# Kernel tuning notes

Measured on AMD Instinct MI355X. Metric: run time of the kernel, lower is better.

## Reference

```python
import jax, jax.numpy as jnp
import numpy as np

B, L, H, NH = 4, 1024, 768, 12      # docs, seq len, hidden, attn heads
E, M, P = 30, 8, 512                # entities/doc, mentions/entity, ht pairs/doc
NLAB = 97                           # DocRED relation count
EMB, BLK = 768, 64                  # emb_size, block_size
OFFSET = 1                          # bert cls offset


def setup_inputs() -> dict:
    key = jax.random.key(0)
    ks = jax.random.split(key, 24)
    def n(k, shp, s=0.02):
        return jax.random.normal(k, shp, jnp.float32) * s
    seq_out = jax.random.normal(ks[0], (B, L, H), jnp.float32)
    attn = jax.random.uniform(ks[1], (B, NH, L, L), jnp.float32)
    mention_idx = jax.random.randint(ks[2], (B, E, M), 0, L - 2)
    ht_pairs = jax.random.randint(ks[3], (B, P, 2), 0, E)
    label_emb = jax.random.normal(ks[4], (NLAB, H), jnp.float32)
    adj = (jax.random.uniform(ks[5], (NLAB, NLAB)) < 0.2).astype(jnp.int32)
    label_adj = jnp.maximum(adj, jnp.eye(NLAB, dtype=jnp.int32))  # self loops
    return dict(
        seq_out=seq_out, attn=attn, mention_idx=mention_idx, ht_pairs=ht_pairs,
        label_adj=label_adj, label_emb=label_emb,
        gW0=n(ks[6], (H, 2 * 500)), gal0=n(ks[7], (2, 500)), gar0=n(ks[8], (2, 500)),
        gW1=n(ks[9], (1000, 2 * 500)), gal1=n(ks[10], (2, 500)), gar1=n(ks[11], (2, 500)),
        gW2=n(ks[12], (1000, H)), gal2=n(ks[13], (1, H)), gar2=n(ks[14], (1, H)),
        ln_gamma=jnp.ones((NLAB,), jnp.float32), ln_beta=jnp.zeros((NLAB,), jnp.float32),
        W_lin2=n(ks[15], (2 * NLAB, NLAB)), b_lin2=jnp.zeros((NLAB,), jnp.float32),
        W_head=n(ks[16], (2 * H, EMB)), b_head=jnp.zeros((EMB,), jnp.float32),
        W_tail=n(ks[17], (2 * H, EMB)), b_tail=jnp.zeros((EMB,), jnp.float32),
        W_bil=n(ks[18], (EMB * BLK + NLAB, NLAB)), b_bil=jnp.zeros((NLAB,), jnp.float32),
    )


def _gat_layer(x, W, al, ar, adj, act):
    nh, od = al.shape
    z = (x @ W).reshape(x.shape[0], nh, od)          # [N, nh, od]
    el = (z * al[None]).sum(-1)                      # src scores [N, nh]
    er = (z * ar[None]).sum(-1)                      # dst scores [N, nh]
    e = jax.nn.leaky_relu(er[:, None, :] + el[None, :, :], 0.2)  # [dst, src, nh]
    e = jnp.where((adj.T > 0)[:, :, None], e, -1e9)
    a = jax.nn.softmax(e, axis=1)
    out = jnp.einsum('vuh,uhd->vhd', a, z)
    return act(out) if act is not None else out


def _layer_norm(x, g, b, eps=1e-5):
    m = x.mean(-1, keepdims=True)
    v = ((x - m) ** 2).mean(-1, keepdims=True)
    return (x - m) * jax.lax.rsqrt(v + eps) * g + b


def _forward(seq_out, attn, label_emb, gW0, gal0, gar0, gW1, gal1, gar1,
             gW2, gal2, gar2, ln_gamma, ln_beta, W_lin2, b_lin2,
             W_head, b_head, W_tail, b_tail, W_bil, b_bil,
             mention_idx, ht_pairs, label_adj):
    pos = mention_idx + OFFSET                                   # [B,E,M]
    bidx3 = jnp.arange(B)[:, None, None]
    ment_emb = seq_out[bidx3, pos]                               # [B,E,M,H]
    ent_emb = jax.nn.logsumexp(ment_emb, axis=2)                 # [B,E,H]
    ment_att = attn[bidx3, :, pos]                               # [B,E,M,NH,L]
    ent_att = ment_att.mean(2)                                   # [B,E,NH,L]

    bidx2 = jnp.arange(B)[:, None]
    h_idx, t_idx = ht_pairs[..., 0], ht_pairs[..., 1]            # [B,P]
    hs = ent_emb[bidx2, h_idx]                                   # [B,P,H]
    ts = ent_emb[bidx2, t_idx]
    ht_att = (ent_att[bidx2, h_idx] * ent_att[bidx2, t_idx]).mean(2)  # [B,P,L]
    ht_att = ht_att / (ht_att.sum(-1, keepdims=True) + 1e-5)
    rs = jnp.einsum('bld,brl->brd', seq_out, ht_att)             # [B,P,H]

    N = B * P
    hs, ts, rs = hs.reshape(N, H), ts.reshape(N, H), rs.reshape(N, H)

    # label GAT: 2 hidden layers (2 heads, concat) + output head
    x = _gat_layer(label_emb, gW0, gal0, gar0, label_adj, None).reshape(NLAB, -1)
    x = jax.nn.elu(x)
    x = _gat_layer(x, gW1, gal1, gar1, label_adj, None).reshape(NLAB, -1)
    x = jax.nn.elu(x)
    lab = _gat_layer(x, gW2, gal2, gar2, label_adj, None).reshape(NLAB, H)

    hs_li = _layer_norm(hs @ lab.T, ln_gamma, ln_beta)           # [N,97]
    ts_li = _layer_norm(ts @ lab.T, ln_gamma, ln_beta)
    logits_li = jnp.concatenate([hs_li, ts_li], axis=1) @ W_lin2 + b_lin2

    hs2 = jnp.tanh(jnp.concatenate([hs, rs], axis=1) @ W_head + b_head)
    ts2 = jnp.tanh(jnp.concatenate([ts, rs], axis=1) @ W_tail + b_tail)
    b1 = hs2.reshape(N, EMB // BLK, BLK)
    b2 = ts2.reshape(N, EMB // BLK, BLK)
    bl = (b1[:, :, :, None] * b2[:, :, None, :]).reshape(N, EMB * BLK)
    logits = jnp.concatenate([bl, logits_li], axis=1) @ W_bil + b_bil
    return logits


def reference(seq_out, attn, mention_idx, ht_pairs, label_adj, label_emb,
              gW0, gal0, gar0, gW1, gal1, gar1, gW2, gal2, gar2,
              ln_gamma, ln_beta, W_lin2, b_lin2, W_head, b_head,
              W_tail, b_tail, W_bil, b_bil):
    return _forward(seq_out, attn, label_emb, gW0, gal0, gar0, gW1, gal1, gar1,
                    gW2, gal2, gar2, ln_gamma, ln_beta, W_lin2, b_lin2,
                    W_head, b_head, W_tail, b_tail, W_bil, b_bil,
                    mention_idx, ht_pairs, label_adj)
```

## Files before the change

### kernel.cpp

```cpp
#include <hip/hip_runtime.h>
#include <hip/hip_bf16.h>
#include <math.h>

typedef __hip_bfloat16 bf16;

__device__ __forceinline__ float toF(float x){ return x; }
__device__ __forceinline__ float toF(bf16 x){ return __bfloat162float(x); }
__device__ __forceinline__ void storeF(float v, float* p){ *p = v; }
__device__ __forceinline__ void storeF(float v, bf16* p){ *p = __float2bfloat16(v); }

__device__ __forceinline__ float bfLo(unsigned u){ return __uint_as_float(u << 16); }
__device__ __forceinline__ float bfHi(unsigned u){ return __uint_as_float(u & 0xFFFF0000u); }

__device__ __forceinline__ bool gateOff(const int* flag, int want){
    return flag && (*flag != want);
}

__global__ void detect_kernel(const unsigned int* gamma_bits, int* flag){
    if (threadIdx.x == 0) *flag = (gamma_bits[0] == 0x3F800000u) ? 0 : 1;
}

template<typename T>
__global__ void cvt_in(const T* __restrict__ in, float* __restrict__ out, int n,
                       const int* flag, int want){
    if (gateOff(flag, want)) return;
    int i = blockIdx.x*256 + threadIdx.x;
    if (i < n) out[i] = toF(in[i]);
}

template<typename T>
__global__ void store_out(const float* __restrict__ in, T* __restrict__ out, int n,
                          const int* flag, int want){
    if (gateOff(flag, want)) return;
    int i = blockIdx.x*256 + threadIdx.x;
    if (i < n) storeF(in[i], &out[i]);
}

template<typename T>
__global__ void ent_emb_kernel(const T* __restrict__ seq, const int* __restrict__ midx,
                               float* __restrict__ ent_emb, const int* flag, int want){
    if (gateOff(flag, want)) return;
    int be = blockIdx.x;
    int b  = be / 30;
    __shared__ int pos[8];
    if (threadIdx.x < 8) pos[threadIdx.x] = midx[be*8 + threadIdx.x] + 1;
    __syncthreads();
    for (int h = threadIdx.x; h < 768; h += 256){
        float v[8], mx = -1e30f;
        #pragma unroll
        for (int m=0;m<8;m++){
            v[m] = toF(seq[((size_t)b*1024 + pos[m])*768 + h]);
            mx = fmaxf(mx, v[m]);
        }
        float s = 0.f;
        #pragma unroll
        for (int m=0;m<8;m++) s += __expf(v[m]-mx);
        ent_emb[(size_t)be*768 + h] = mx + __logf(s);
    }
}

template<typename T>
__global__ void ent_att_kernel(const T* __restrict__ attn, const int* __restrict__ midx,
                               float* __restrict__ ent_att, const int* flag, int want){
    if (gateOff(flag, want)) return;
    int id = blockIdx.x;
    int nh = id % 12, be = id / 12, b = be / 30;
    __shared__ int pos[8];
    if (threadIdx.x < 8) pos[threadIdx.x] = midx[be*8 + threadIdx.x] + 1;
    __syncthreads();
    const size_t base = ((size_t)(b*12 + nh))*1024*1024;
    for (int l = threadIdx.x; l < 1024; l += 256){
        float s = 0.f;
        #pragma unroll
        for (int m=0;m<8;m++) s += toF(attn[base + (size_t)pos[m]*1024 + l]);
        ent_att[((size_t)be*12 + nh)*1024 + l] = s * 0.125f;
    }
}

__global__ void pair_kernel(const float* __restrict__ ent_emb, const float* __restrict__ ent_att,
                            const int* __restrict__ htp,
                            float* __restrict__ hs, float* __restrict__ ts, float* __restrict__ ht_att){
    int n = blockIdx.x;
    int b = n >> 9;
    int h = htp[n*2], t = htp[n*2+1];
    const float* eh = ent_emb + ((size_t)b*30 + h)*768;
    const float* et = ent_emb + ((size_t)b*30 + t)*768;
    for (int d = threadIdx.x; d < 768; d += 256){
        hs[(size_t)n*768 + d] = eh[d];
        ts[(size_t)n*768 + d] = et[d];
    }
    const float* ah = ent_att + ((size_t)b*30 + h)*12*1024;
    const float* at = ent_att + ((size_t)b*30 + t)*12*1024;
    float loc[4]; float psum = 0.f;
    #pragma unroll
    for (int i=0;i<4;i++){
        int l = threadIdx.x + i*256;
        float s = 0.f;
        #pragma unroll
        for (int k=0;k<12;k++) s += ah[k*1024 + l]*at[k*1024 + l];
        s *= (1.f/12.f);
        loc[i] = s; psum += s;
    }
    __shared__ float red[256];
    red[threadIdx.x] = psum; __syncthreads();
    for (int off=128; off>0; off>>=1){
        if (threadIdx.x < off) red[threadIdx.x] += red[threadIdx.x+off];
        __syncthreads();
    }
    float inv = 1.f/(red[0] + 1e-5f);
    #pragma unroll
    for (int i=0;i<4;i++){
        int l = threadIdx.x + i*256;
        ht_att[(size_t)n*1024 + l] = loc[i]*inv;
    }
}

template<typename T>
__global__ void rs_kernel(const T* __restrict__ seq, const float* __restrict__ ht_att,
                          float* __restrict__ rs, const int* flag, int want){
    if (gateOff(flag, want)) return;
    int hc = blockIdx.x;
    int pt = blockIdx.y;
    int b  = blockIdx.z;
    int h  = hc*256 + threadIdx.x;
    float acc[16];
    #pragma unroll
    for (int i=0;i<16;i++) acc[i]=0.f;
    __shared__ __align__(16) float att[64][20];
    for (int l0=0; l0<1024; l0+=64){
        for (int idx=threadIdx.x; idx<1024; idx+=256){
            int pl = idx>>6, lo = idx&63;
            att[lo][pl] = ht_att[((size_t)(b*512 + pt*16 + pl))*1024 + l0 + lo];
        }
        __syncthreads();
        for (int lo=0; lo<64; lo++){
            float sv = toF(seq[((size_t)b*1024 + l0 + lo)*768 + h]);
            #pragma unroll
            for (int p=0;p<16;p++) acc[p] += att[lo][p]*sv;
        }
        __syncthreads();
    }
    #pragma unroll
    for (int p=0;p<16;p++)
        rs[((size_t)(b*512 + pt*16 + p))*768 + h] = acc[p];
}

template<typename TB>
__global__ __launch_bounds__(256) void gemm64(const float* __restrict__ A1, const float* __restrict__ A2,
                                              int K1, int K, const TB* __restrict__ B,
                                              const TB* __restrict__ bias, int act,
                                              float* __restrict__ C, int M, int N,
                                              const int* flag, int want){
    if (gateOff(flag, want)) return;
    __shared__ __align__(16) float As[32][68];
    __shared__ __align__(16) float Bs[32][68];
    int m0 = blockIdx.y*64, n0 = blockIdx.x*64;
    int tid = threadIdx.x;
    int tr = tid>>4, tc = tid&15;
    float acc[4][4];
    #pragma unroll
    for (int i=0;i<4;i++)
        #pragma unroll
        for (int j=0;j<4;j++) acc[i][j]=0.f;
    int K2 = K - K1;
    for (int k0=0; k0<K; k0+=32){
        for (int e=tid; e<2048; e+=256){
            int k=e&31, m=e>>5;
            int gm=m0+m, gk=k0+k;
            float v=0.f;
            if (gm<M && gk<K) v = (gk<K1)? A1[(size_t)gm*K1+gk] : A2[(size_t)gm*K2 + (gk-K1)];
            As[k][m]=v;
        }
        for (int e=tid; e<2048; e+=256){
            int nn=e&63, k=e>>6;
            int gk=k0+k, gn=n0+nn;
            float v=0.f;
            if (gk<K && gn<N) v = toF(B[(size_t)gk*N+gn]);
            Bs[k][nn]=v;
        }
        __syncthreads();
        #pragma unroll
        for (int kk=0;kk<32;kk++){
            float4 a4 = *(const float4*)&As[kk][tr<<2];
            float4 b4 = *(const float4*)&Bs[kk][tc<<2];
            float av[4]={a4.x,a4.y,a4.z,a4.w}, bv[4]={b4.x,b4.y,b4.z,b4.w};
            #pragma unroll
            for (int i=0;i<4;i++)
                #pragma unroll
                for (int j=0;j<4;j++) acc[i][j] += av[i]*bv[j];
        }
        __syncthreads();
    }
    #pragma unroll
    for (int i=0;i<4;i++){
        int m = m0 + (tr<<2) + i;
        if (m >= M) continue;
        #pragma unroll
        for (int j=0;j<4;j++){
            int n = n0 + (tc<<2) + j;
            if (n >= N) continue;
            float v = acc[i][j];
            if (bias) v += toF(bias[n]);
            if (act == 1) v = tanhf(v);
            C[(size_t)m*N + n] = v;
        }
    }
}

template<typename T>
__global__ void elr_kernel(const float* __restrict__ z, const T* __restrict__ al,
                           const T* __restrict__ ar, int nh, int od,
                           float* __restrict__ el, float* __restrict__ er,
                           const int* flag, int want){
    if (gateOff(flag, want)) return;
    int u = blockIdx.x;
    __shared__ float sl[256], sr[256];
    int tid = threadIdx.x;
    for (int h=0; h<nh; h++){
        float a=0.f, r=0.f;
        for (int d=tid; d<od; d+=256){
            float zz = z[((size_t)u*nh + h)*od + d];
            a += zz*toF(al[h*od+d]);
            r += zz*toF(ar[h*od+d]);
        }
        sl[tid]=a; sr[tid]=r; __syncthreads();
        for (int off=128; off>0; off>>=1){
            if (tid<off){ sl[tid]+=sl[tid+off]; sr[tid]+=sr[tid+off]; }
            __syncthreads();
        }
        if (tid==0){ el[u*nh+h]=sl[0]; er[u*nh+h]=sr[0]; }
        __syncthreads();
    }
}

__global__ void gat_agg_kernel(const float* __restrict__ z, const float* __restrict__ el,
                               const float* __restrict__ er, const int* __restrict__ adj,
                               int nh, int od, int applyElu, float* __restrict__ out){
    int v = blockIdx.x;
    int tid = threadIdx.x;
    __shared__ float e[2][97];
    int D = nh*od;
    for (int idx=tid; idx<97*nh; idx+=256){
        int u = idx % 97, h = idx / 97;
        float ev;
        if (adj[u*97 + v] > 0){
            ev = er[v*nh+h] + el[u*nh+h];
            ev = ev > 0.f ? ev : 0.2f*ev;
        } else ev = -1e9f;
        e[h][u] = ev;
    }
    __syncthreads();
    if (tid < nh){
        float mx=-1e30f;
        for (int u2=0;u2<97;u2++) mx = fmaxf(mx, e[tid][u2]);
        float s=0.f;
        for (int u2=0;u2<97;u2++){ float x=__expf(e[tid][u2]-mx); e[tid][u2]=x; s+=x; }
        float inv = 1.f/s;
        for (int u2=0;u2<97;u2++) e[tid][u2]*=inv;
    }
    __syncthreads();
    for (int d0=tid; d0<D; d0+=256){
        int h = d0 / od;
        float s = 0.f;
        for (int u2=0;u2<97;u2++) s += e[h][u2]*z[(size_t)u2*D + d0];
        if (applyElu) s = s>0.f ? s : expm1f(s);
        out[(size_t)v*D + d0] = s;
    }
}

__global__ void transpose_kernel(const float* __restrict__ lab, float* __restrict__ labT){
    int i = blockIdx.x*256 + threadIdx.x;
    if (i < 97*768){ int c = i/768, k = i%768; labT[(size_t)k*97 + c] = lab[i]; }
}

template<typename T>
__global__ void ln_kernel(const float* __restrict__ in, const T* __restrict__ gamma,
                          const T* __restrict__ beta, float* __restrict__ out,
                          const int* flag, int want){
    if (gateOff(flag, want)) return;
    int n = blockIdx.x;
    int tid = threadIdx.x;
    __shared__ float red[128];
    float v = (tid < 97) ? in[(size_t)n*97 + tid] : 0.f;
    red[tid] = v; __syncthreads();
    for (int off=64; off>0; off>>=1){
        if (tid<off) red[tid]+=red[tid+off];
        __syncthreads();
    }
    float mean = red[0]*(1.f/97.f); __syncthreads();
    float d = (tid < 97) ? v - mean : 0.f;
    red[tid] = d*d; __syncthreads();
    for (int off=64; off>0; off>>=1){
        if (tid<off) red[tid]+=red[tid+off];
        __syncthreads();
    }
    float rstd = rsqrtf(red[0]*(1.f/97.f) + 1e-5f);
    if (tid < 97)
        out[(size_t)n*97 + tid] = d*rstd*toF(gamma[tid]) + toF(beta[tid]);
}

template<typename T>
__global__ __launch_bounds__(256) void bilinear_kernel(const float* __restrict__ hs2,
                                                       const float* __restrict__ ts2,
                                                       const T* __restrict__ Wb,
                                                       float* __restrict__ out,
                                                       const int* flag, int want){
    if (gateOff(flag, want)) return;
    int nb = blockIdx.x, g = blockIdx.y, ih = blockIdx.z;
    int n0 = nb*32;
    __shared__ __align__(16) float hsb[16][36];
    __shared__ __align__(16) float tsb[64][36];
    __shared__ __align__(16) float wbuf[2][3104];
    int tid = threadIdx.x;
    for (int e=tid; e<512; e+=256){
        int i = e&15, nl = e>>4;
        hsb[i][nl] = hs2[(size_t)(n0+nl)*768 + g*64 + ih*16 + i];
    }
    for (int e=tid; e<2048; e+=256){
        int j = e&63, nl = e>>6;
        tsb[j][nl] = ts2[(size_t)(n0+nl)*768 + g*64 + j];
    }
    const T* Wg = Wb + (size_t)g*4096*97 + (size_t)ih*16*6208;

    if constexpr (sizeof(T) == 4){
        const float4* src = (const float4*)Wg;
        float4* dst = (float4*)wbuf[0];
        #pragma unroll
        for (int u=0;u<4;u++){ int e = tid + u*256; if (e < 776) dst[e] = src[e]; }
    } else {
        const uint4* src = (const uint4*)Wg;
        #pragma unroll
        for (int u=0;u<2;u++){
            int e = tid + u*256;
            if (e < 388){
                uint4 w = src[e];
                float* d = &wbuf[0][e*8];
                d[0]=bfLo(w.x); d[1]=bfHi(w.x); d[2]=bfLo(w.y); d[3]=bfHi(w.y);
                d[4]=bfLo(w.z); d[5]=bfHi(w.z); d[6]=bfLo(w.w); d[7]=bfHi(w.w);
            }
        }
    }
    __syncthreads();

    int cg = tid & 63;
    int ng = tid >> 6;
    int c0 = cg, c1 = cg + 64;
    bool c1ok = (c1 < 97);
    float acc0[8], acc1[8];
    #pragma unroll
    for (int q=0;q<8;q++){ acc0[q]=0.f; acc1[q]=0.f; }

    int cur = 0;
    for (int k=0; k<32; ++k){
        int i = k>>1;
        float4 wreg[4];
        uint4  breg[2];
        if (k+1 < 32){
            if constexpr (sizeof(T) == 4){
                const float4* src = (const float4*)(Wg + (size_t)(k+1)*3104);
                #pragma unroll
                for (int u=0;u<4;u++){ int e = tid + u*256; if (e < 776) wreg[u] = src[e]; }
            } else {
                const uint4* src = (const uint4*)(Wg + (size_t)(k+1)*3104);
                #pragma unroll
                for (int u=0;u<2;u++){ int e = tid + u*256; if (e < 388) breg[u] = src[e]; }
            }
        }
        float a[8];
        #pragma unroll
        for (int q=0;q<8;q++) a[q] = hsb[i][ng*8+q];
        float s0[8], s1[8];
        #pragma unroll
        for (int q=0;q<8;q++){ s0[q]=0.f; s1[q]=0.f; }
        const float* wrow = wbuf[cur];
        int jbase = (k&1)*32;
        #pragma unroll 2
        for (int j=0;j<32;j++){
            float w0 = wrow[j*97 + c0];
            float w1 = c1ok ? wrow[j*97 + c1] : 0.f;
            const float4* tp = (const float4*)&tsb[jbase + j][ng*8];
            float4 t0 = tp[0], t1 = tp[1];
            float tv[8] = {t0.x,t0.y,t0.z,t0.w,t1.x,t1.y,t1.z,t1.w};
            #pragma unroll
            for (int q=0;q<8;q++){ s0[q] += tv[q]*w0; s1[q] += tv[q]*w1; }
        }
        #pragma unroll
        for (int q=0;q<8;q++){ acc0[q] += a[q]*s0[q]; acc1[q] += a[q]*s1[q]; }
        if (k+1 < 32){
            if constexpr (sizeof(T) == 4){
                float4* dst = (float4*)wbuf[cur^1];
                #pragma unroll
                for (int u=0;u<4;u++){ int e = tid + u*256; if (e < 776) dst[e] = wreg[u]; }
            } else {
                float* base = wbuf[cur^1];
                #pragma unroll
                for (int u=0;u<2;u++){
                    int e = tid + u*256;
                    if (e < 388){
                        uint4 w = breg[u];
                        float* d = &base[e*8];
                        d[0]=bfLo(w.x); d[1]=bfHi(w.x); d[2]=bfLo(w.y); d[3]=bfHi(w.y);
                        d[4]=bfLo(w.z); d[5]=bfHi(w.z); d[6]=bfLo(w.w); d[7]=bfHi(w.w);
                    }
                }
            }
        }
        __syncthreads();
        cur ^= 1;
    }
    #pragma unroll
    for (int q=0;q<8;q++){
        int n = n0 + ng*8 + q;
        atomicAdd(&out[(size_t)n*97 + c0], acc0[q]);
        if (c1ok) atomicAdd(&out[(size_t)n*97 + c1], acc1[q]);
    }
}

extern "C" void kernel_launch(void* const* d_in, const int* in_sizes, int n_in,
                              void* d_out, int out_size, void* d_ws, size_t ws_size,
                              hipStream_t stream){
    (void)in_sizes; (void)n_in; (void)ws_size; (void)out_size;
    const void* seq   = d_in[0];
    const void* attn  = d_in[1];
    const int*  midx  = (const int*)d_in[2];
    const int*  htp   = (const int*)d_in[3];
    const int*  adj   = (const int*)d_in[4];
    const void* lemb  = d_in[5];
    const void* gW0   = d_in[6];
    const void* gal0  = d_in[7];
    const void* gar0  = d_in[8];
    const void* gW1   = d_in[9];
    const void* gal1  = d_in[10];
    const void* gar1  = d_in[11];
    const void* gW2   = d_in[12];
    const void* gal2  = d_in[13];
    const void* gar2  = d_in[14];
    const void* ln_g  = d_in[15];
    const void* ln_b  = d_in[16];
    const void* Wlin2 = d_in[17];
    const void* blin2 = d_in[18];
    const void* Whead = d_in[19];
    const void* bhead = d_in[20];
    const void* Wtail = d_in[21];
    const void* btail = d_in[22];
    const void* Wbil  = d_in[23];
    const void* bbil  = d_in[24];

    int*   flag = (int*)d_ws;
    float* base = (float*)d_ws + 16;
    float* hs     = base;
    float* ts     = hs + 1572864;
    float* R2     = ts + 1572864;
    float* ht_att = R2;
    float* hs2    = R2;
    float* li_raw = R2 + 1572864;
    float* R3     = R2 + 2097152;
    float* ent_emb= R3;
    float* ent_att= R3 + 92160;
    float* li     = R3;
    float* ts2    = R3;
    float* rs     = R3 + 1572864;
    float* sm     = rs + 1572864;
    float* x0   = sm;
    float* zbuf = x0 + 74496;
    float* x1   = zbuf + 97000;
    float* x2   = x1 + 97000;
    float* lab  = x2 + 97000;
    float* labT = lab + 74496;
    float* el   = labT + 74496;
    float* er   = el + 194;
    float* ll   = er + 194;
    float* logits = ll + 198656;

    detect_kernel<<<1,64,0,stream>>>((const unsigned int*)ln_g, flag);

    ent_emb_kernel<float><<<120,256,0,stream>>>((const float*)seq, midx, ent_emb, flag, 0);
    ent_emb_kernel<bf16 ><<<120,256,0,stream>>>((const bf16* )seq, midx, ent_emb, flag, 1);
    ent_att_kernel<float><<<1440,256,0,stream>>>((const float*)attn, midx, ent_att, flag, 0);
    ent_att_kernel<bf16 ><<<1440,256,0,stream>>>((const bf16* )attn, midx, ent_att, flag, 1);
    pair_kernel<<<2048,256,0,stream>>>(ent_emb, ent_att, htp, hs, ts, ht_att);
    rs_kernel<float><<<dim3(3,32,4),256,0,stream>>>((const float*)seq, ht_att, rs, flag, 0);
    rs_kernel<bf16 ><<<dim3(3,32,4),256,0,stream>>>((const bf16* )seq, ht_att, rs, flag, 1);

    cvt_in<float><<<(74496+255)/256,256,0,stream>>>((const float*)lemb, x0, 74496, flag, 0);
    cvt_in<bf16 ><<<(74496+255)/256,256,0,stream>>>((const bf16* )lemb, x0, 74496, flag, 1);

    auto gemm_pair = [&](const float* A1, const float* A2, int K1, int K,
                         const void* B, const void* bias, int act,
                         float* C, int M, int N, dim3 grid){
        gemm64<float><<<grid,256,0,stream>>>(A1,A2,K1,K,(const float*)B,(const float*)bias,act,C,M,N,flag,0);
        gemm64<bf16 ><<<grid,256,0,stream>>>(A1,A2,K1,K,(const bf16* )B,(const bf16* )bias,act,C,M,N,flag,1);
    };
    auto elr_pair = [&](const float* z, const void* al, const void* ar, int nh, int od){
        elr_kernel<float><<<97,256,0,stream>>>(z,(const float*)al,(const float*)ar,nh,od,el,er,flag,0);
        elr_kernel<bf16 ><<<97,256,0,stream>>>(z,(const bf16* )al,(const bf16* )ar,nh,od,el,er,flag,1);
    };

    gemm_pair(x0, nullptr, 768, 768, gW0, nullptr, 0, zbuf, 97, 1000, dim3(16,2));
    elr_pair(zbuf, gal0, gar0, 2, 500);
    gat_agg_kernel<<<97,256,0,stream>>>(zbuf, el, er, adj, 2, 500, 1, x1);
    gemm_pair(x1, nullptr, 1000, 1000, gW1, nullptr, 0, zbuf, 97, 1000, dim3(16,2));
    elr_pair(zbuf, gal1, gar1, 2, 500);
    gat_agg_kernel<<<97,256,0,stream>>>(zbuf, el, er, adj, 2, 500, 1, x2);
    gemm_pair(x2, nullptr, 1000, 1000, gW2, nullptr, 0, zbuf, 97, 768, dim3(12,2));
    elr_pair(zbuf, gal2, gar2, 1, 768);
    gat_agg_kernel<<<97,256,0,stream>>>(zbuf, el, er, adj, 1, 768, 0, lab);
    transpose_kernel<<<(74496+255)/256,256,0,stream>>>(lab, labT);

    gemm64<float><<<dim3(2,64),256,0,stream>>>(hs, nullptr, 768, 768, labT,
        (const float*)nullptr, 0, li_raw, 4096, 97, nullptr, 0);
    ln_kernel<float><<<4096,128,0,stream>>>(li_raw, (const float*)ln_g, (const float*)ln_b, li, flag, 0);
    ln_kernel<bf16 ><<<4096,128,0,stream>>>(li_raw, (const bf16* )ln_g, (const bf16* )ln_b, li, flag, 1);
    gemm_pair(li, li + 2048*97, 97, 194, Wlin2, blin2, 0, ll, 2048, 97, dim3(2,32));

    gemm_pair(hs, rs, 768, 1536, Whead, bhead, 1, hs2, 2048, 768, dim3(12,32));
    gemm_pair(ts, rs, 768, 1536, Wtail, btail, 1, ts2, 2048, 768, dim3(12,32));

    gemm64<float><<<dim3(2,32),256,0,stream>>>(ll, nullptr, 97, 97,
        (const float*)Wbil + (size_t)49152*97, (const float*)bbil, 0, logits, 2048, 97, flag, 0);
    gemm64<bf16 ><<<dim3(2,32),256,0,stream>>>(ll, nullptr, 97, 97,
        (const bf16* )Wbil + (size_t)49152*97, (const bf16* )bbil, 0, logits, 2048, 97, flag, 1);

    bilinear_kernel<float><<<dim3(64,12,4),256,0,stream>>>(hs2, ts2, (const float*)Wbil, logits, flag, 0);
    bilinear_kernel<bf16 ><<<dim3(64,12,4),256,0,stream>>>(hs2, ts2, (const bf16* )Wbil, logits, flag, 1);

    store_out<float><<<(198656+255)/256,256,0,stream>>>(logits, (float*)d_out, 198656, flag, 0);
    store_out<bf16 ><<<(198656+255)/256,256,0,stream>>>(logits, (bf16*)d_out, 198656, flag, 1);
}
```

Before: 2.623 ms.

## Compute head/tail and label projections per entity, merge dtype kernel pairs

Because hs and ts are gathers of per-entity embeddings, the entity-side parts of the head/tail GEMMs and the label-interaction GEMM plus LayerNorm and lin2 are now computed once per entity (120 rows) rather than per pair (2048 or 4096 rows). Per-pair results are then assembled by gathering them, either in the GEMM epilogue (a new act==2 path that adds the gathered entity term before tanh) or in a small ll kernel. The separate float and bf16 kernel launches are also merged into single kernels that branch on the dtype flag at runtime. This removes redundant FLOPs, the hs/ts materialization and about half of the launches, in exchange for more code size and a possible register-pressure increase from instantiating both templates in each kernel.

```diff
diff --git a/kernel.cpp b/kernel.cpp
--- a/kernel.cpp
+++ b/kernel.cpp
@@ -6,89 +6,90 @@
 
 __device__ __forceinline__ float toF(float x){ return x; }
 __device__ __forceinline__ float toF(bf16 x){ return __bfloat162float(x); }
-__device__ __forceinline__ void storeF(float v, float* p){ *p = v; }
-__device__ __forceinline__ void storeF(float v, bf16* p){ *p = __float2bfloat16(v); }
 
 __device__ __forceinline__ float bfLo(unsigned u){ return __uint_as_float(u << 16); }
 __device__ __forceinline__ float bfHi(unsigned u){ return __uint_as_float(u & 0xFFFF0000u); }
 
-__device__ __forceinline__ bool gateOff(const int* flag, int want){
-    return flag && (*flag != want);
-}
+__device__ __forceinline__ int rdFlag(const int* flag){ return flag ? *flag : 0; }
 
 __global__ void detect_kernel(const unsigned int* gamma_bits, int* flag){
     if (threadIdx.x == 0) *flag = (gamma_bits[0] == 0x3F800000u) ? 0 : 1;
 }
 
 template<typename T>
-__global__ void cvt_in(const T* __restrict__ in, float* __restrict__ out, int n,
-                       const int* flag, int want){
-    if (gateOff(flag, want)) return;
+__device__ __forceinline__ void cvt_core(const T* in, float* out, int n){
     int i = blockIdx.x*256 + threadIdx.x;
     if (i < n) out[i] = toF(in[i]);
 }
-
-template<typename T>
-__global__ void store_out(const float* __restrict__ in, T* __restrict__ out, int n,
-                          const int* flag, int want){
-    if (gateOff(flag, want)) return;
+__global__ void cvt_in_m(const void* in, float* __restrict__ out, int n, const int* flag){
+    if (!rdFlag(flag)) cvt_core<float>((const float*)in, out, n);
+    else               cvt_core<bf16 >((const bf16* )in, out, n);
+}
+
+template<typename T>
+__device__ __forceinline__ void store_core(const float* in, T* out, int n){
     int i = blockIdx.x*256 + threadIdx.x;
-    if (i < n) storeF(in[i], &out[i]);
-}
-
-template<typename T>
-__global__ void ent_emb_kernel(const T* __restrict__ seq, const int* __restrict__ midx,
-                               float* __restrict__ ent_emb, const int* flag, int want){
-    if (gateOff(flag, want)) return;
-    int be = blockIdx.x;
-    int b  = be / 30;
+    if (i < n) out[i] = (sizeof(T)==4) ? (T)in[i] : (T)__float2bfloat16(in[i]);
+}
+__global__ void store_out_m(const float* __restrict__ in, void* out, int n, const int* flag){
+    if (!rdFlag(flag)){ int i = blockIdx.x*256 + threadIdx.x; if (i<n) ((float*)in, ((float*)out)[i] = in[i]); }
+    else              { int i = blockIdx.x*256 + threadIdx.x; if (i<n) ((bf16*)out)[i] = __float2bfloat16(in[i]); }
+}
+
+template<typename T>
+__device__ __forceinline__ void ent_emb_core(const T* seq, const int* pos, int b, int be,
+                                             float* ent_emb){
+    for (int h = threadIdx.x; h < 768; h += 256){
+        float v[8], mx = -1e30f;
+        #pragma unroll
+        for (int m=0;m<8;m++){
+            v[m] = toF(seq[((size_t)b*1024 + pos[m])*768 + h]);
+            mx = fmaxf(mx, v[m]);
+        }
+        float s = 0.f;
+        #pragma unroll
+        for (int m=0;m<8;m++) s += __expf(v[m]-mx);
+        ent_emb[(size_t)be*768 + h] = mx + __logf(s);
+    }
+}
+__global__ void ent_emb_m(const void* seq, const int* __restrict__ midx,
+                          float* __restrict__ ent_emb, const int* flag){
+    int be = blockIdx.x, b = be/30;
     __shared__ int pos[8];
     if (threadIdx.x < 8) pos[threadIdx.x] = midx[be*8 + threadIdx.x] + 1;
     __syncthreads();
-    for (int h = threadIdx.x; h < 768; h += 256){
-        float v[8], mx = -1e30f;
-        #pragma unroll
-        for (int m=0;m<8;m++){
-            v[m] = toF(seq[((size_t)b*1024 + pos[m])*768 + h]);
-            mx = fmaxf(mx, v[m]);
-        }
+    if (!rdFlag(flag)) ent_emb_core<float>((const float*)seq, pos, b, be, ent_emb);
+    else               ent_emb_core<bf16 >((const bf16* )seq, pos, b, be, ent_emb);
+}
+
+template<typename T>
+__device__ __forceinline__ void ent_att_core(const T* attn, const int* pos, size_t base,
+                                             int be, int nh, float* ent_att){
+    for (int l = threadIdx.x; l < 1024; l += 256){
         float s = 0.f;
         #pragma unroll
-        for (int m=0;m<8;m++) s += __expf(v[m]-mx);
-        ent_emb[(size_t)be*768 + h] = mx + __logf(s);
-    }
-}
-
-template<typename T>
-__global__ void ent_att_kernel(const T* __restrict__ attn, const int* __restrict__ midx,
-                               float* __restrict__ ent_att, const int* flag, int want){
-    if (gateOff(flag, want)) return;
+        for (int m=0;m<8;m++) s += toF(attn[base + (size_t)pos[m]*1024 + l]);
+        ent_att[((size_t)be*12 + nh)*1024 + l] = s * 0.125f;
+    }
+}
+__global__ void ent_att_m(const void* attn, const int* __restrict__ midx,
+                          float* __restrict__ ent_att, const int* flag){
     int id = blockIdx.x;
     int nh = id % 12, be = id / 12, b = be / 30;
     __shared__ int pos[8];
     if (threadIdx.x < 8) pos[threadIdx.x] = midx[be*8 + threadIdx.x] + 1;
     __syncthreads();
     const size_t base = ((size_t)(b*12 + nh))*1024*1024;
-    for (int l = threadIdx.x; l < 1024; l += 256){
-        float s = 0.f;
-        #pragma unroll
-        for (int m=0;m<8;m++) s += toF(attn[base + (size_t)pos[m]*1024 + l]);
-        ent_att[((size_t)be*12 + nh)*1024 + l] = s * 0.125f;
-    }
-}
-
-__global__ void pair_kernel(const float* __restrict__ ent_emb, const float* __restrict__ ent_att,
+    if (!rdFlag(flag)) ent_att_core<float>((const float*)attn, pos, base, be, nh, ent_att);
+    else               ent_att_core<bf16 >((const bf16* )attn, pos, base, be, nh, ent_att);
+}
+
+__global__ void pair_kernel(const float* __restrict__ ent_att,
                             const int* __restrict__ htp,
-                            float* __restrict__ hs, float* __restrict__ ts, float* __restrict__ ht_att){
+                            float* __restrict__ ht_att){
     int n = blockIdx.x;
     int b = n >> 9;
     int h = htp[n*2], t = htp[n*2+1];
-    const float* eh = ent_emb + ((size_t)b*30 + h)*768;
-    const float* et = ent_emb + ((size_t)b*30 + t)*768;
-    for (int d = threadIdx.x; d < 768; d += 256){
-        hs[(size_t)n*768 + d] = eh[d];
-        ts[(size_t)n*768 + d] = et[d];
-    }
     const float* ah = ent_att + ((size_t)b*30 + h)*12*1024;
     const float* at = ent_att + ((size_t)b*30 + t)*12*1024;
     float loc[4]; float psum = 0.f;
@@ -116,17 +117,13 @@
 }
 
 template<typename T>
-__global__ void rs_kernel(const T* __restrict__ seq, const float* __restrict__ ht_att,
-                          float* __restrict__ rs, const int* flag, int want){
-    if (gateOff(flag, want)) return;
-    int hc = blockIdx.x;
-    int pt = blockIdx.y;
-    int b  = blockIdx.z;
+__device__ __forceinline__ void rs_core(const T* seq, const float* ht_att, float* rs,
+                                        float (*att)[20]){
+    int hc = blockIdx.x, pt = blockIdx.y, b = blockIdx.z;
     int h  = hc*256 + threadIdx.x;
     float acc[16];
     #pragma unroll
     for (int i=0;i<16;i++) acc[i]=0.f;
-    __shared__ __align__(16) float att[64][20];
     for (int l0=0; l0<1024; l0+=64){
         for (int idx=threadIdx.x; idx<1024; idx+=256){
             int pl = idx>>6, lo = idx&63;
@@ -144,16 +141,19 @@
     for (int p=0;p<16;p++)
         rs[((size_t)(b*512 + pt*16 + p))*768 + h] = acc[p];
 }
+__global__ void rs_m(const void* seq, const float* __restrict__ ht_att,
+                     float* __restrict__ rs, const int* flag){
+    __shared__ __align__(16) float att[64][20];
+    if (!rdFlag(flag)) rs_core<float>((const float*)seq, ht_att, rs, att);
+    else               rs_core<bf16 >((const bf16* )seq, ht_att, rs, att);
+}
 
 template<typename TB>
-__global__ __launch_bounds__(256) void gemm64(const float* __restrict__ A1, const float* __restrict__ A2,
-                                              int K1, int K, const TB* __restrict__ B,
-                                              const TB* __restrict__ bias, int act,
-                                              float* __restrict__ C, int M, int N,
-                                              const int* flag, int want){
-    if (gateOff(flag, want)) return;
-    __shared__ __align__(16) float As[32][68];
-    __shared__ __align__(16) float Bs[32][68];
+__device__ __forceinline__ void gemm64_core(const float* A1, const float* A2,
+                                            int K1, int K, const TB* B, const TB* bias,
+                                            int act, float* C, int M, int N,
+                                            const float* addG, const int* htp, int sel,
+                                            float (*As)[68], float (*Bs)[68]){
     int m0 = blockIdx.y*64, n0 = blockIdx.x*64;
     int tid = threadIdx.x;
     int tr = tid>>4, tc = tid&15;
@@ -195,6 +195,8 @@
     for (int i=0;i<4;i++){
         int m = m0 + (tr<<2) + i;
         if (m >= M) continue;
+        int e2 = (act==2) ? htp[m*2+sel] : 0;
+        int bb = m >> 9;
         #pragma unroll
         for (int j=0;j<4;j++){
             int n = n0 + (tc<<2) + j;
@@ -202,19 +204,32 @@
             float v = acc[i][j];
             if (bias) v += toF(bias[n]);
             if (act == 1) v = tanhf(v);
+            else if (act == 2) v = tanhf(v + addG[(size_t)(bb*30+e2)*768 + n]);
             C[(size_t)m*N + n] = v;
         }
     }
 }
-
-template<typename T>
-__global__ void elr_kernel(const float* __restrict__ z, const T* __restrict__ al,
-                           const T* __restrict__ ar, int nh, int od,
-                           float* __restrict__ el, float* __restrict__ er,
-                           const int* flag, int want){
-    if (gateOff(flag, want)) return;
+__global__ __launch_bounds__(256) void gemm64_m(const float* __restrict__ A1,
+                                                const float* __restrict__ A2,
+                                                int K1, int K, const void* B, size_t boff,
+                                                const void* bias, int act,
+                                                float* __restrict__ C, int M, int N,
+                                                const int* flag,
+                                                const float* __restrict__ addG,
+                                                const int* __restrict__ htp, int sel){
+    __shared__ __align__(16) float As[32][68];
+    __shared__ __align__(16) float Bs[32][68];
+    if (!rdFlag(flag))
+        gemm64_core<float>(A1,A2,K1,K,(const float*)B + boff,(const float*)bias,act,C,M,N,addG,htp,sel,As,Bs);
+    else
+        gemm64_core<bf16 >(A1,A2,K1,K,(const bf16* )B + boff,(const bf16* )bias,act,C,M,N,addG,htp,sel,As,Bs);
+}
+
+template<typename T>
+__device__ __forceinline__ void elr_core(const float* z, const T* al, const T* ar,
+                                         int nh, int od, float* el, float* er,
+                                         float* sl, float* sr){
     int u = blockIdx.x;
-    __shared__ float sl[256], sr[256];
     int tid = threadIdx.x;
     for (int h=0; h<nh; h++){
         float a=0.f, r=0.f;
@@ -231,6 +246,13 @@
         if (tid==0){ el[u*nh+h]=sl[0]; er[u*nh+h]=sr[0]; }
         __syncthreads();
     }
+}
+__global__ void elr_m(const float* __restrict__ z, const void* al, const void* ar,
+                      int nh, int od, float* __restrict__ el, float* __restrict__ er,
+                      const int* flag){
+    __shared__ float sl[256], sr[256];
+    if (!rdFlag(flag)) elr_core<float>(z,(const float*)al,(const float*)ar,nh,od,el,er,sl,sr);
+    else               elr_core<bf16 >(z,(const bf16* )al,(const bf16* )ar,nh,od,el,er,sl,sr);
 }
 
 __global__ void gat_agg_kernel(const float* __restrict__ z, const float* __restrict__ el,
@@ -274,14 +296,11 @@
 }
 
 template<typename T>
-__global__ void ln_kernel(const float* __restrict__ in, const T* __restrict__ gamma,
-                          const T* __restrict__ beta, float* __restrict__ out,
-                          const int* flag, int want){
-    if (gateOff(flag, want)) return;
-    int n = blockIdx.x;
-    int tid = threadIdx.x;
-    __shared__ float red[128];
-    float v = (tid < 97) ? in[(size_t)n*97 + tid] : 0.f;
+__device__ __forceinline__ void p5_core(const float* EL, const T* g, const T* bta,
+                                        const T* W2, float* Eh2, float* Et2,
+                                        float* red, float* eln){
+    int e = blockIdx.x, tid = threadIdx.x;
+    float v = (tid < 97) ? EL[(size_t)e*97 + tid] : 0.f;
     red[tid] = v; __syncthreads();
     for (int off=64; off>0; off>>=1){
         if (tid<off) red[tid]+=red[tid+off];
@@ -295,22 +314,53 @@
         __syncthreads();
     }
     float rstd = rsqrtf(red[0]*(1.f/97.f) + 1e-5f);
-    if (tid < 97)
-        out[(size_t)n*97 + tid] = d*rstd*toF(gamma[tid]) + toF(beta[tid]);
-}
-
-template<typename T>
-__global__ __launch_bounds__(256) void bilinear_kernel(const float* __restrict__ hs2,
-                                                       const float* __restrict__ ts2,
-                                                       const T* __restrict__ Wb,
-                                                       float* __restrict__ out,
-                                                       const int* flag, int want){
-    if (gateOff(flag, want)) return;
+    if (tid < 97) eln[tid] = d*rstd*toF(g[tid]) + toF(bta[tid]);
+    __syncthreads();
+    if (tid < 97){
+        float s0=0.f, s1=0.f;
+        for (int k=0;k<97;k++){
+            float x = eln[k];
+            s0 += x*toF(W2[k*97 + tid]);
+            s1 += x*toF(W2[(k+97)*97 + tid]);
+        }
+        Eh2[(size_t)e*97 + tid] = s0;
+        Et2[(size_t)e*97 + tid] = s1;
+    }
+}
+__global__ void p5_m(const float* __restrict__ EL, const void* g, const void* bta,
+                     const void* W2, float* __restrict__ Eh2, float* __restrict__ Et2,
+                     const int* flag){
+    __shared__ float red[128];
+    __shared__ float eln[97];
+    if (!rdFlag(flag)) p5_core<float>(EL,(const float*)g,(const float*)bta,(const float*)W2,Eh2,Et2,red,eln);
+    else               p5_core<bf16 >(EL,(const bf16* )g,(const bf16* )bta,(const bf16* )W2,Eh2,Et2,red,eln);
+}
+
+template<typename T>
+__device__ __forceinline__ void ll_core(const float* Eh2, const float* Et2,
+                                        const int* htp, const T* blin2, float* ll){
+    int n = blockIdx.x;
+    int b = n >> 9;
+    int h = htp[n*2], t = htp[n*2+1];
+    int c = threadIdx.x;
+    if (c < 97)
+        ll[(size_t)n*97 + c] = Eh2[(size_t)(b*30+h)*97 + c]
+                             + Et2[(size_t)(b*30+t)*97 + c] + toF(blin2[c]);
+}
+__global__ void ll_m(const float* __restrict__ Eh2, const float* __restrict__ Et2,
+                     const int* __restrict__ htp, const void* blin2,
+                     float* __restrict__ ll, const int* flag){
+    if (!rdFlag(flag)) ll_core<float>(Eh2,Et2,htp,(const float*)blin2,ll);
+    else               ll_core<bf16 >(Eh2,Et2,htp,(const bf16* )blin2,ll);
+}
+
+template<typename T>
+__device__ __forceinline__ void bilinear_core(const float* hs2, const float* ts2,
+                                              const T* Wb, float* out,
+                                              float (*hsb)[36], float (*tsb)[36],
+                                              float (*wbuf)[3104]){
     int nb = blockIdx.x, g = blockIdx.y, ih = blockIdx.z;
     int n0 = nb*32;
-    __shared__ __align__(16) float hsb[16][36];
-    __shared__ __align__(16) float tsb[64][36];
-    __shared__ __align__(16) float wbuf[2][3104];
     int tid = threadIdx.x;
     for (int e=tid; e<512; e+=256){
         int i = e&15, nl = e>>4;
@@ -322,7 +372,7 @@
     }
     const T* Wg = Wb + (size_t)g*4096*97 + (size_t)ih*16*6208;
 
-    if constexpr (sizeof(T) == 4){
+    if (sizeof(T) == 4){
         const float4* src = (const float4*)Wg;
         float4* dst = (float4*)wbuf[0];
         #pragma unroll
@@ -356,7 +406,7 @@
         float4 wreg[4];
         uint4  breg[2];
         if (k+1 < 32){
-            if constexpr (sizeof(T) == 4){
+            if (sizeof(T) == 4){
                 const float4* src = (const float4*)(Wg + (size_t)(k+1)*3104);
                 #pragma unroll
                 for (int u=0;u<4;u++){ int e = tid + u*256; if (e < 776) wreg[u] = src[e]; }
@@ -387,7 +437,7 @@
         #pragma unroll
         for (int q=0;q<8;q++){ acc0[q] += a[q]*s0[q]; acc1[q] += a[q]*s1[q]; }
         if (k+1 < 32){
-            if constexpr (sizeof(T) == 4){
+            if (sizeof(T) == 4){
                 float4* dst = (float4*)wbuf[cur^1];
                 #pragma unroll
                 for (int u=0;u<4;u++){ int e = tid + u*256; if (e < 776) dst[e] = wreg[u]; }
@@ -414,6 +464,17 @@
         atomicAdd(&out[(size_t)n*97 + c0], acc0[q]);
         if (c1ok) atomicAdd(&out[(size_t)n*97 + c1], acc1[q]);
     }
+}
+__global__ __launch_bounds__(256) void bilinear_m(const float* __restrict__ hs2,
+                                                  const float* __restrict__ ts2,
+                                                  const void* Wb,
+                                                  float* __restrict__ out,
+                                                  const int* flag){
+    __shared__ __align__(16) float hsb[16][36];
+    __shared__ __align__(16) float tsb[64][36];
+    __shared__ __align__(16) float wbuf[2][3104];
+    if (!rdFlag(flag)) bilinear_core<float>(hs2, ts2, (const float*)Wb, out, hsb, tsb, wbuf);
+    else               bilinear_core<bf16 >(hs2, ts2, (const bf16* )Wb, out, hsb, tsb, wbuf);
 }
 
 extern "C" void kernel_launch(void* const* d_in, const int* in_sizes, int n_in,
@@ -448,19 +509,20 @@
 
     int*   flag = (int*)d_ws;
     float* base = (float*)d_ws + 16;
-    float* hs     = base;
-    float* ts     = hs + 1572864;
-    float* R2     = ts + 1572864;
+    float* EWh  = base;
+    float* EWt  = EWh + 92160;
+    float* EL   = EWt + 92160;
+    float* Eh2  = EL  + 11640;
+    float* Et2  = Eh2 + 11640;
+    float* R2     = base + 2*1572864;
     float* ht_att = R2;
     float* hs2    = R2;
-    float* li_raw = R2 + 1572864;
     float* R3     = R2 + 2097152;
     float* ent_emb= R3;
     float* ent_att= R3 + 92160;
-    float* li     = R3;
     float* ts2    = R3;
     float* rs     = R3 + 1572864;
-    float* sm     = rs + 1572864;
+    float* sm   = rs + 1572864;
     float* x0   = sm;
     float* zbuf = x0 + 74496;
     float* x1   = zbuf + 97000;
@@ -474,56 +536,45 @@
 
     detect_kernel<<<1,64,0,stream>>>((const unsigned int*)ln_g, flag);
 
-    ent_emb_kernel<float><<<120,256,0,stream>>>((const float*)seq, midx, ent_emb, flag, 0);
-    ent_emb_kernel<bf16 ><<<120,256,0,stream>>>((const bf16* )seq, midx, ent_emb, flag, 1);
-    ent_att_kernel<float><<<1440,256,0,stream>>>((const float*)attn, midx, ent_att, flag, 0);
-    ent_att_kernel<bf16 ><<<1440,256,0,stream>>>((const bf16* )attn, midx, ent_att, flag, 1);
-    pair_kernel<<<2048,256,0,stream>>>(ent_emb, ent_att, htp, hs, ts, ht_att);
-    rs_kernel<float><<<dim3(3,32,4),256,0,stream>>>((const float*)seq, ht_att, rs, flag, 0);
-    rs_kernel<bf16 ><<<dim3(3,32,4),256,0,stream>>>((const bf16* )seq, ht_att, rs, flag, 1);
-
-    cvt_in<float><<<(74496+255)/256,256,0,stream>>>((const float*)lemb, x0, 74496, flag, 0);
-    cvt_in<bf16 ><<<(74496+255)/256,256,0,stream>>>((const bf16* )lemb, x0, 74496, flag, 1);
-
-    auto gemm_pair = [&](const float* A1, const float* A2, int K1, int K,
-                         const void* B, const void* bias, int act,
-                         float* C, int M, int N, dim3 grid){
-        gemm64<float><<<grid,256,0,stream>>>(A1,A2,K1,K,(const float*)B,(const float*)bias,act,C,M,N,flag,0);
-        gemm64<bf16 ><<<grid,256,0,stream>>>(A1,A2,K1,K,(const bf16* )B,(const bf16* )bias,act,C,M,N,flag,1);
-    };
-    auto elr_pair = [&](const float* z, const void* al, const void* ar, int nh, int od){
-        elr_kernel<float><<<97,256,0,stream>>>(z,(const float*)al,(const float*)ar,nh,od,el,er,flag,0);
-        elr_kernel<bf16 ><<<97,256,0,stream>>>(z,(const bf16* )al,(const bf16* )ar,nh,od,el,er,flag,1);
-    };
-
-    gemm_pair(x0, nullptr, 768, 768, gW0, nullptr, 0, zbuf, 97, 1000, dim3(16,2));
-    elr_pair(zbuf, gal0, gar0, 2, 500);
+    ent_emb_m<<<120,256,0,stream>>>(seq, midx, ent_emb, flag);
+    ent_att_m<<<1440,256,0,stream>>>(attn, midx, ent_att, flag);
+    pair_kernel<<<2048,256,0,stream>>>(ent_att, htp, ht_att);
+    rs_m<<<dim3(3,32,4),256,0,stream>>>(seq, ht_att, rs, flag);
+
+    gemm64_m<<<dim3(12,2),256,0,stream>>>(ent_emb, nullptr, 768, 768, Whead, 0, bhead, 0,
+                                          EWh, 120, 768, flag, nullptr, nullptr, 0);
+    gemm64_m<<<dim3(12,2),256,0,stream>>>(ent_emb, nullptr, 768, 768, Wtail, 0, btail, 0,
+                                          EWt, 120, 768, flag, nullptr, nullptr, 0);
+
+    cvt_in_m<<<(74496+255)/256,256,0,stream>>>(lemb, x0, 74496, flag);
+
+    gemm64_m<<<dim3(16,2),256,0,stream>>>(x0, nullptr, 768, 768, gW0, 0, nullptr, 0,
+                                          zbuf, 97, 1000, flag, nullptr, nullptr, 0);
+    elr_m<<<97,256,0,stream>>>(zbuf, gal0, gar0, 2, 500, el, er, flag);
     gat_agg_kernel<<<97,256,0,stream>>>(zbuf, el, er, adj, 2, 500, 1, x1);
-    gemm_pair(x1, nullptr, 1000, 1000, gW1, nullptr, 0, zbuf, 97, 1000, dim3(16,2));
-    elr_pair(zbuf, gal1, gar1, 2, 500);
+    gemm64_m<<<dim3(16,2),256,0,stream>>>(x1, nullptr, 1000, 1000, gW1, 0, nullptr, 0,
+                                          zbuf, 97, 1000, flag, nullptr, nullptr, 0);
+    elr_m<<<97,256,0,stream>>>(zbuf, gal1, gar1, 2, 500, el, er, flag);
     gat_agg_kernel<<<97,256,0,stream>>>(zbuf, el, er, adj, 2, 500, 1, x2);
-    gemm_pair(x2, nullptr, 1000, 1000, gW2, nullptr, 0, zbuf, 97, 768, dim3(12,2));
-    elr_pair(zbuf, gal2, gar2, 1, 768);
+    gemm64_m<<<dim3(12,2),256,0,stream>>>(x2, nullptr, 1000, 1000, gW2, 0, nullptr, 0,
+                                          zbuf, 97, 768, flag, nullptr, nullptr, 0);
+    elr_m<<<97,256,0,stream>>>(zbuf, gal2, gar2, 1, 768, el, er, flag);
     gat_agg_kernel<<<97,256,0,stream>>>(zbuf, el, er, adj, 1, 768, 0, lab);
     transpose_kernel<<<(74496+255)/256,256,0,stream>>>(lab, labT);
 
-    gemm64<float><<<dim3(2,64),256,0,stream>>>(hs, nullptr, 768, 768, labT,
-        (const float*)nullptr, 0, li_raw, 4096, 97, nullptr, 0);
-    ln_kernel<float><<<4096,128,0,stream>>>(li_raw, (const float*)ln_g, (const float*)ln_b, li, flag, 0);
-    ln_kernel<bf16 ><<<4096,128,0,stream>>>(li_raw, (const bf16* )ln_g, (const bf16* )ln_b, li, flag, 1);
-    gemm_pair(li, li + 2048*97, 97, 194, Wlin2, blin2, 0, ll, 2048, 97, dim3(2,32));
-
-    gemm_pair(hs, rs, 768, 1536, Whead, bhead, 1, hs2, 2048, 768, dim3(12,32));
-    gemm_pair(ts, rs, 768, 1536, Wtail, btail, 1, ts2, 2048, 768, dim3(12,32));
-
-    gemm64<float><<<dim3(2,32),256,0,stream>>>(ll, nullptr, 97, 97,
-        (const float*)Wbil + (size_t)49152*97, (const float*)bbil, 0, logits, 2048, 97, flag, 0);
-    gemm64<bf16 ><<<dim3(2,32),256,0,stream>>>(ll, nullptr, 97, 97,
-        (const bf16* )Wbil + (size_t)49152*97, (const bf16* )bbil, 0, logits, 2048, 97, flag, 1);
-
-    bilinear_kernel<float><<<dim3(64,12,4),256,0,stream>>>(hs2, ts2, (const float*)Wbil, logits, flag, 0);
-    bilinear_kernel<bf16 ><<<dim3(64,12,4),256,0,stream>>>(hs2, ts2, (const bf16* )Wbil, logits, flag, 1);
-
-    store_out<float><<<(198656+255)/256,256,0,stream>>>(logits, (float*)d_out, 198656, flag, 0);
-    store_out<bf16 ><<<(198656+255)/256,256,0,stream>>>(logits, (bf16*)d_out, 198656, flag, 1);
-}
+    gemm64_m<<<dim3(2,2),256,0,stream>>>(ent_emb, nullptr, 768, 768, labT, 0, nullptr, 0,
+                                         EL, 120, 97, nullptr, nullptr, nullptr, 0);
+    p5_m<<<120,128,0,stream>>>(EL, ln_g, ln_b, Wlin2, Eh2, Et2, flag);
+    ll_m<<<2048,128,0,stream>>>(Eh2, Et2, htp, blin2, ll, flag);
+
+    gemm64_m<<<dim3(12,32),256,0,stream>>>(rs, nullptr, 768, 768, Whead, 589824, nullptr, 2,
+                                           hs2, 2048, 768, flag, EWh, htp, 0);
+    gemm64_m<<<dim3(12,32),256,0,stream>>>(rs, nullptr, 768, 768, Wtail, 589824, nullptr, 2,
+                                           ts2, 2048, 768, flag, EWt, htp, 1);
+
+    gemm64_m<<<dim3(2,32),256,0,stream>>>(ll, nullptr, 97, 97, Wbil, (size_t)49152*97, bbil, 0,
+                                          logits, 2048, 97, flag, nullptr, nullptr, 0);
+    bilinear_m<<<dim3(64,12,4),256,0,stream>>>(hs2, ts2, Wbil, logits, flag);
+
+    store_out_m<<<(198656+255)/256,256,0,stream>>>(logits, d_out, 198656, flag);
+}
```

Measured after the change: 2.580 ms. Within noise of the previous version (-1.6%).
